# Performance work log

Hardware: AMD Instinct MI355X
Metric: run time of the kernel (lower is better)

## Reference

```python
import jax, jax.numpy as jnp
import numpy as np

B, S, D, E, H, K = 2, 2048, 1024, 8, 4096, 2


def setup_inputs() -> dict:
    key = jax.random.key(0)
    ks = jax.random.split(key, 7)
    sd = 1.0 / np.sqrt(D)
    sh = 1.0 / np.sqrt(H)
    return {
        "x": jax.random.normal(ks[0], (B, S, D), dtype=jnp.float32),
        "router_w": jax.random.uniform(ks[1], (D, E), jnp.float32, -sd, sd),
        "router_b": jnp.zeros((E,), jnp.float32),
        "w1": jax.random.uniform(ks[2], (E, D, H), jnp.float32, -sd, sd),
        "b1": jnp.zeros((E, H), jnp.float32),
        "w2": jax.random.uniform(ks[3], (E, H, D), jnp.float32, -sh, sh),
        "b2": jnp.zeros((E, D), jnp.float32),
    }


def reference(x, router_w, router_b, w1, b1, w2, b2):
    # Router: softmax over experts, then top-k and renormalize
    router_logits = jnp.einsum("bsd,de->bse", x, router_w) + router_b
    router_probs = jax.nn.softmax(router_logits, axis=-1)
    top_k_probs, top_k_indices = jax.lax.top_k(router_probs, K)  # [B,S,K]
    top_k_probs = top_k_probs / jnp.sum(top_k_probs, axis=-1, keepdims=True)

    # Dense all-expert FFN (Block assumed: Linear -> GELU -> Linear)
    h = jax.nn.gelu(jnp.einsum("bsd,edh->bseh", x, w1) + b1)  # [B,S,E,H]
    expert_outputs = jnp.einsum("bseh,ehd->bsed", h, w2) + b2  # [B,S,E,D]

    # Gather top-k experts per token and combine with renormalized probs
    idx = top_k_indices[..., None]  # [B,S,K,1]
    selected = jnp.take_along_axis(expert_outputs, idx, axis=2)  # [B,S,K,D]
    return jnp.sum(selected * top_k_probs[..., None], axis=2)  # [B,S,D]
```

## Files before the change

### kernel.cpp

```cpp
#include <hip/hip_runtime.h>
#include <hip/hip_bf16.h>

#define TOK   4096
#define DDIM  1024
#define NEXP  8
#define HDIM  4096
#define KSEL  2
#define NPAIR (TOK * KSEL)

typedef __attribute__((ext_vector_type(8))) _Float16 f16x8;
typedef __attribute__((ext_vector_type(4))) _Float16 f16x4;
typedef __attribute__((ext_vector_type(4))) float    f32x4;

__device__ __forceinline__ void gload16(const void* g, void* l) {
  __builtin_amdgcn_global_load_lds((const __attribute__((address_space(1))) void*)g,
                                   (__attribute__((address_space(3))) void*)l, 16, 0, 0);
}

__device__ __forceinline__ float gelu_tanh(float u) {
  float inner = 0.7978845608028654f * (u + 0.044715f * u * u * u);
  float t2 = __expf(2.f * inner);
  return u - u / (t2 + 1.f);
}

__global__ __launch_bounds__(256) void k_router(const float* __restrict__ x,
    const float* __restrict__ rw, const float* __restrict__ rb,
    int* __restrict__ tidx, float* __restrict__ tw, int* __restrict__ counts,
    _Float16* __restrict__ xb) {
  const int t    = blockIdx.x * 4 + (threadIdx.x >> 6);
  const int lane = threadIdx.x & 63;
  const float* xr = x + (size_t)t * DDIM;
  _Float16*   xbr = xb + (size_t)t * DDIM;
  float acc[NEXP];
#pragma unroll
  for (int e = 0; e < NEXP; ++e) acc[e] = 0.f;
  for (int d0 = lane * 4; d0 < DDIM; d0 += 256) {
    const float4 xv = *(const float4*)(xr + d0);
    f16x4 hx;
    hx[0] = (_Float16)xv.x; hx[1] = (_Float16)xv.y;
    hx[2] = (_Float16)xv.z; hx[3] = (_Float16)xv.w;
    *(f16x4*)(xbr + d0) = hx;
#pragma unroll
    for (int i = 0; i < 4; ++i) {
      const float xs = (&xv.x)[i];
      const float4 r0 = *(const float4*)(rw + (size_t)(d0 + i) * NEXP);
      const float4 r1 = *(const float4*)(rw + (size_t)(d0 + i) * NEXP + 4);
      acc[0] += xs * r0.x; acc[1] += xs * r0.y; acc[2] += xs * r0.z; acc[3] += xs * r0.w;
      acc[4] += xs * r1.x; acc[5] += xs * r1.y; acc[6] += xs * r1.z; acc[7] += xs * r1.w;
    }
  }
#pragma unroll
  for (int e = 0; e < NEXP; ++e) {
    float v = acc[e];
#pragma unroll
    for (int s = 32; s; s >>= 1) v += __shfl_xor(v, s, 64);
    acc[e] = v;
  }
  if (lane == 0) {
    float lg[NEXP];
#pragma unroll
    for (int e = 0; e < NEXP; ++e) lg[e] = acc[e] + rb[e];
    int i0 = 0;
#pragma unroll
    for (int e = 1; e < NEXP; ++e) if (lg[e] > lg[i0]) i0 = e;
    int i1 = -1; float best = -3.4e38f;
#pragma unroll
    for (int e = 0; e < NEXP; ++e) {
      if (e == i0) continue;
      if (lg[e] > best) { best = lg[e]; i1 = e; }
    }
    float w0 = 1.f / (1.f + expf(lg[i1] - lg[i0]));
    tidx[t * 2]     = i0;  tidx[t * 2 + 1] = i1;
    tw[t * 2]       = w0;  tw[t * 2 + 1]   = 1.f - w0;
    atomicAdd(&counts[i0], 1);
    atomicAdd(&counts[i1], 1);
  }
}

__global__ __launch_bounds__(1024) void k_scan(const int* __restrict__ tidx,
                       const float* __restrict__ tw,
                       const int* __restrict__ counts, int* __restrict__ offs,
                       int* __restrict__ row_token, float* __restrict__ row_w,
                       int* __restrict__ inv) {
  __shared__ int soff[NEXP + 1];
  __shared__ int scur[NEXP];
  if (threadIdx.x == 0) {
    int run = 0;
    for (int e = 0; e < NEXP; ++e) { soff[e] = run; run += counts[e]; }
    soff[NEXP] = run;
    for (int e = 0; e <= NEXP; ++e) offs[e] = soff[e];
  }
  __syncthreads();
  if (threadIdx.x < NEXP) scur[threadIdx.x] = soff[threadIdx.x];
  __syncthreads();
  const int lane = threadIdx.x & 63;
#pragma unroll
  for (int it = 0; it < NPAIR / 1024; ++it) {
    const int p = it * 1024 + threadIdx.x;
    const int e = tidx[p];
    int pos = 0;
#pragma unroll
    for (int ee = 0; ee < NEXP; ++ee) {
      unsigned long long m = __ballot(e == ee);
      if (!m) continue;
      int base = 0;
      if (lane == 0) base = atomicAdd(&scur[ee], __popcll(m));
      base = __shfl(base, 0, 64);
      if (e == ee) pos = base + __popcll(m & ((1ull << lane) - 1ull));
    }
    row_token[pos] = p >> 1;
    row_w[pos]     = tw[p];
    inv[p]         = pos;
  }
}

__global__ __launch_bounds__(256) void k_transpose(const float* __restrict__ in,
    _Float16* __restrict__ out, int Rr, int Cc) {
  __shared__ _Float16 tile[64][72];
  const size_t esz = (size_t)Rr * Cc;
  const float* ip = in + esz * blockIdx.z;
  _Float16*    op = out + esz * blockIdx.z;
  const int i0 = blockIdx.y * 64;
  const int j0 = blockIdx.x * 64;
  const int tx = threadIdx.x & 15, ty = threadIdx.x >> 4;
#pragma unroll
  for (int rr = 0; rr < 4; ++rr) {
    int r = ty + rr * 16;
    float4 v = *(const float4*)(ip + (size_t)(i0 + r) * Cc + j0 + tx * 4);
    tile[r][tx * 4 + 0] = (_Float16)v.x;
    tile[r][tx * 4 + 1] = (_Float16)v.y;
    tile[r][tx * 4 + 2] = (_Float16)v.z;
    tile[r][tx * 4 + 3] = (_Float16)v.w;
  }
  __syncthreads();
#pragma unroll
  for (int cc = 0; cc < 4; ++cc) {
    int c = ty + cc * 16;
    f16x4 o;
#pragma unroll
    for (int k = 0; k < 4; ++k) o[k] = tile[tx * 4 + k][c];
    *(f16x4*)(op + (size_t)(j0 + c) * Rr + i0 + tx * 4) = o;
  }
}

#define BM 128
#define BN 128
#define BKK 32


__global__ __launch_bounds__(256) void k_gemm1(
    const _Float16* __restrict__ xb,
    const _Float16* __restrict__ w1t,
    const float* __restrict__ b1,
    const int* __restrict__ offs,
    const int* __restrict__ row_token,
    _Float16* __restrict__ hbuf) {
  const int e    = blockIdx.z;
  const int off0 = offs[e];
  const int ne   = offs[e + 1] - off0;
  const int m0   = blockIdx.y * BM;
  if (m0 >= ne) return;
  const int n0   = blockIdx.x * BN;
  const int mrem = ne - m0;

  __shared__ __align__(16) char smem[32768];

  const int tid = threadIdx.x;
  const int wv = tid >> 6, lane = tid & 63;
  const int l15 = lane & 15;
  const int wr = wv >> 1, wc = wv & 1;

  const int rA0 = (wv * 2 + 0) * 16 + (lane >> 2);
  const int rA1 = (wv * 2 + 1) * 16 + (lane >> 2);
  const char* a_c = (const char*)xb;
  const char* b_c = (const char*)(w1t + (size_t)e * HDIM * DDIM);
  const int rc0 = (rA0 < mrem) ? rA0 : (mrem - 1);
  const int rc1 = (rA1 < mrem) ? rA1 : (mrem - 1);
  const char* ap0 = a_c + (size_t)row_token[off0 + m0 + rc0] * (DDIM * 2)
                        + (((lane & 3) ^ ((rA0 >> 1) & 3)) << 4);
  const char* ap1 = a_c + (size_t)row_token[off0 + m0 + rc1] * (DDIM * 2)
                        + (((lane & 3) ^ ((rA1 >> 1) & 3)) << 4);
  const char* bp0 = b_c + (size_t)(n0 + rA0) * (DDIM * 2)
                        + (((lane & 3) ^ ((rA0 >> 1) & 3)) << 4);
  const char* bp1 = b_c + (size_t)(n0 + rA1) * (DDIM * 2)
                        + (((lane & 3) ^ ((rA1 >> 1) & 3)) << 4);
  char* ldsA0 = smem + (wv * 2 + 0) * 1024;
  char* ldsA1 = smem + (wv * 2 + 1) * 1024;
  char* ldsB0 = smem + 16384 + (wv * 2 + 0) * 1024;
  char* ldsB1 = smem + 16384 + (wv * 2 + 1) * 1024;

  const unsigned foff = (unsigned)(((lane >> 4) ^ ((l15 >> 1) & 3)) << 4);

  f32x4 acc[4][4] = {};
  const int NT = DDIM / BKK;

  gload16(ap0, ldsA0); gload16(ap1, ldsA1);
  gload16(bp0, ldsB0); gload16(bp1, ldsB1);

#pragma unroll 2
  for (int ks = 0; ks < NT; ++ks) {
    const int cur = ks & 1;
    if (ks + 1 < NT) {
      const int nb = (cur ^ 1) * 8192;
      const size_t kb = (size_t)(ks + 1) * 64;
      gload16(ap0 + kb, ldsA0 + nb); gload16(ap1 + kb, ldsA1 + nb);
      gload16(bp0 + kb, ldsB0 + nb); gload16(bp1 + kb, ldsB1 + nb);
      asm volatile("s_waitcnt vmcnt(4)" ::: "memory");
    } else {
      asm volatile("s_waitcnt vmcnt(0)" ::: "memory");
    }
    __builtin_amdgcn_sched_barrier(0);
    __builtin_amdgcn_s_barrier();
    const char* Ab = smem + cur * 8192;
    const char* Bb = smem + 16384 + cur * 8192;
    f16x8 af[4], bfr[4];
#pragma unroll
    for (int m = 0; m < 4; ++m)
      af[m] = *(const f16x8*)(Ab + (wr * 64 + m * 16 + l15) * 64 + foff);
#pragma unroll
    for (int n = 0; n < 4; ++n)
      bfr[n] = *(const f16x8*)(Bb + (wc * 64 + n * 16 + l15) * 64 + foff);
#pragma unroll
    for (int m = 0; m < 4; ++m)
#pragma unroll
      for (int n = 0; n < 4; ++n)
        acc[m][n] = __builtin_amdgcn_mfma_f32_16x16x32_f16(af[m], bfr[n], acc[m][n], 0, 0, 0);
    __builtin_amdgcn_sched_barrier(0);
    __builtin_amdgcn_s_barrier();
  }

  float bias[4];
#pragma unroll
  for (int n = 0; n < 4; ++n)
    bias[n] = b1[(size_t)e * HDIM + n0 + wc * 64 + n * 16 + l15];
#pragma unroll
  for (int m = 0; m < 4; ++m) {
#pragma unroll
    for (int j = 0; j < 4; ++j) {
      int row = wr * 64 + m * 16 + (lane >> 4) * 4 + j;
#pragma unroll
      for (int n = 0; n < 4; ++n) {
        int col = wc * 64 + n * 16 + l15;
        *(_Float16*)(smem + (row << 8) + (((col << 1) ^ ((row & 15) << 4)))) =
            (_Float16)gelu_tanh(acc[m][n][j] + bias[n]);
      }
    }
  }
  __syncthreads();
  {
    const int srow = tid >> 1, half = tid & 1;
    if (srow < mrem) {
      _Float16* hr = hbuf + (size_t)(off0 + m0 + srow) * HDIM + n0 + half * 64;
#pragma unroll
      for (int i = 0; i < 8; ++i) {
        f16x8 v = *(const f16x8*)(smem + (srow << 8) + (((half * 128 + i * 16) ^ ((srow & 15) << 4))));
        *(f16x8*)(hr + i * 8) = v;
      }
    }
  }
}

template <bool YB>
__global__ __launch_bounds__(256) void k_gemm2(
    const _Float16* __restrict__ hbuf,
    const _Float16* __restrict__ w2t,
    const float* __restrict__ b2,
    const int* __restrict__ offs,
    const int* __restrict__ row_token,
    const float* __restrict__ row_w,
    _Float16* __restrict__ yb,
    float* __restrict__ out) {
  const int e    = blockIdx.z >> 1;
  const int kh   = blockIdx.z & 1;
  const int off0 = offs[e];
  const int ne   = offs[e + 1] - off0;
  const int m0   = blockIdx.y * BM;
  if (m0 >= ne) return;
  const int n0   = blockIdx.x * BN;
  const int mrem = ne - m0;

  __shared__ __align__(16) char smem[32768];

  const int tid = threadIdx.x;
  const int wv = tid >> 6, lane = tid & 63;
  const int l15 = lane & 15;
  const int wr = wv >> 1, wc = wv & 1;

  const int rA0 = (wv * 2 + 0) * 16 + (lane >> 2);
  const int rA1 = (wv * 2 + 1) * 16 + (lane >> 2);
  const char* a_c = (const char*)hbuf;
  const char* b_c = (const char*)(w2t + (size_t)e * DDIM * HDIM);
  const int rc0 = (rA0 < mrem) ? rA0 : (mrem - 1);
  const int rc1 = (rA1 < mrem) ? rA1 : (mrem - 1);
  const size_t khb = (size_t)kh * (2048 * 2);
  const char* ap0 = a_c + (size_t)(off0 + m0 + rc0) * (HDIM * 2) + khb
                        + (((lane & 3) ^ ((rA0 >> 1) & 3)) << 4);
  const char* ap1 = a_c + (size_t)(off0 + m0 + rc1) * (HDIM * 2) + khb
                        + (((lane & 3) ^ ((rA1 >> 1) & 3)) << 4);
  const char* bp0 = b_c + (size_t)(n0 + rA0) * (HDIM * 2) + khb
                        + (((lane & 3) ^ ((rA0 >> 1) & 3)) << 4);
  const char* bp1 = b_c + (size_t)(n0 + rA1) * (HDIM * 2) + khb
                        + (((lane & 3) ^ ((rA1 >> 1) & 3)) << 4);
  char* ldsA0 = smem + (wv * 2 + 0) * 1024;
  char* ldsA1 = smem + (wv * 2 + 1) * 1024;
  char* ldsB0 = smem + 16384 + (wv * 2 + 0) * 1024;
  char* ldsB1 = smem + 16384 + (wv * 2 + 1) * 1024;

  const unsigned foff = (unsigned)(((lane >> 4) ^ ((l15 >> 1) & 3)) << 4);

  f32x4 acc[4][4] = {};
  const int NT = 2048 / BKK;

  gload16(ap0, ldsA0); gload16(ap1, ldsA1);
  gload16(bp0, ldsB0); gload16(bp1, ldsB1);

#pragma unroll 2
  for (int ks = 0; ks < NT; ++ks) {
    const int cur = ks & 1;
    if (ks + 1 < NT) {
      const int nb = (cur ^ 1) * 8192;
      const size_t kb = (size_t)(ks + 1) * 64;
      gload16(ap0 + kb, ldsA0 + nb); gload16(ap1 + kb, ldsA1 + nb);
      gload16(bp0 + kb, ldsB0 + nb); gload16(bp1 + kb, ldsB1 + nb);
      asm volatile("s_waitcnt vmcnt(4)" ::: "memory");
    } else {
      asm volatile("s_waitcnt vmcnt(0)" ::: "memory");
    }
    __builtin_amdgcn_sched_barrier(0);
    __builtin_amdgcn_s_barrier();
    const char* Ab = smem + cur * 8192;
    const char* Bb = smem + 16384 + cur * 8192;
    f16x8 af[4], bfr[4];
#pragma unroll
    for (int m = 0; m < 4; ++m)
      af[m] = *(const f16x8*)(Ab + (wr * 64 + m * 16 + l15) * 64 + foff);
#pragma unroll
    for (int n = 0; n < 4; ++n)
      bfr[n] = *(const f16x8*)(Bb + (wc * 64 + n * 16 + l15) * 64 + foff);
#pragma unroll
    for (int m = 0; m < 4; ++m)
#pragma unroll
      for (int n = 0; n < 4; ++n)
        acc[m][n] = __builtin_amdgcn_mfma_f32_16x16x32_f16(af[m], bfr[n], acc[m][n], 0, 0, 0);
    __builtin_amdgcn_sched_barrier(0);
    __builtin_amdgcn_s_barrier();
  }

  if (YB) {
    _Float16* ypart = yb + (size_t)kh * NPAIR * DDIM;
#pragma unroll
    for (int m = 0; m < 4; ++m) {
#pragma unroll
      for (int j = 0; j < 4; ++j) {
        int row = wr * 64 + m * 16 + (lane >> 4) * 4 + j;
#pragma unroll
        for (int n = 0; n < 4; ++n) {
          int col = wc * 64 + n * 16 + l15;
          *(_Float16*)(smem + (row << 8) + (((col << 1) ^ ((row & 15) << 4)))) =
              (_Float16)acc[m][n][j];
        }
      }
    }
    __syncthreads();
    const int srow = tid >> 1, half = tid & 1;
    if (srow < mrem) {
      _Float16* yr = ypart + (size_t)(off0 + m0 + srow) * DDIM + n0 + half * 64;
#pragma unroll
      for (int i = 0; i < 8; ++i) {
        f16x8 v = *(const f16x8*)(smem + (srow << 8) + (((half * 128 + i * 16) ^ ((srow & 15) << 4))));
        *(f16x8*)(yr + i * 8) = v;
      }
    }
  } else {
    float bias[4];
#pragma unroll
    for (int n = 0; n < 4; ++n)
      bias[n] = (kh == 0) ? b2[(size_t)e * DDIM + n0 + wc * 64 + n * 16 + l15] : 0.f;
#pragma unroll
    for (int m = 0; m < 4; ++m) {
#pragma unroll
      for (int j = 0; j < 4; ++j) {
        int row = wr * 64 + m * 16 + (lane >> 4) * 4 + j;
        if (row < mrem) {
          int g = off0 + m0 + row;
          float wgt = row_w[g];
          float* op = out + (size_t)row_token[g] * DDIM + n0 + wc * 64 + l15;
#pragma unroll
          for (int n = 0; n < 4; ++n)
            atomicAdd(op + n * 16, wgt * (acc[m][n][j] + bias[n]));
        }
      }
    }
  }
}

__global__ __launch_bounds__(256) void k_combine(const _Float16* __restrict__ yb,
    const int* __restrict__ inv, const int* __restrict__ tidx,
    const float* __restrict__ tw, const float* __restrict__ b2,
    float* __restrict__ out) {
  const int t  = blockIdx.x * 2 + (threadIdx.x >> 7);
  const int c8 = (threadIdx.x & 127) * 8;
  const int g0 = inv[2 * t],  g1 = inv[2 * t + 1];
  const int e0 = tidx[2 * t], e1 = tidx[2 * t + 1];
  const float w0 = tw[2 * t], w1 = tw[2 * t + 1];
  const _Float16* y1p = yb + (size_t)NPAIR * DDIM;
  f16x8 a0 = *(const f16x8*)(yb  + (size_t)g0 * DDIM + c8);
  f16x8 a1 = *(const f16x8*)(y1p + (size_t)g0 * DDIM + c8);
  f16x8 b0 = *(const f16x8*)(yb  + (size_t)g1 * DDIM + c8);
  f16x8 b1v = *(const f16x8*)(y1p + (size_t)g1 * DDIM + c8);
  float o[8];
#pragma unroll
  for (int i = 0; i < 8; ++i) {
    float bA = b2[(size_t)e0 * DDIM + c8 + i];
    float bB = b2[(size_t)e1 * DDIM + c8 + i];
    o[i] = w0 * ((float)a0[i] + (float)a1[i] + bA) + w1 * ((float)b0[i] + (float)b1v[i] + bB);
  }
  float* op = out + (size_t)t * DDIM + c8;
  *(float4*)op       = make_float4(o[0], o[1], o[2], o[3]);
  *(float4*)(op + 4) = make_float4(o[4], o[5], o[6], o[7]);
}

extern "C" void kernel_launch(void* const* d_in, const int* in_sizes, int n_in,
                              void* d_out, int out_size, void* d_ws, size_t ws_size,
                              hipStream_t stream) {
  const float* x  = (const float*)d_in[0];
  const float* rw = (const float*)d_in[1];
  const float* rb = (const float*)d_in[2];
  const float* w1 = (const float*)d_in[3];
  const float* b1 = (const float*)d_in[4];
  const float* w2 = (const float*)d_in[5];
  const float* b2 = (const float*)d_in[6];
  float* out = (float*)d_out;
  char* ws = (char*)d_ws;

  int*      tidx    = (int*)(ws + 0);
  float*    tw      = (float*)(ws + 32768);
  int*      counts  = (int*)(ws + 65536);
  int*      offs    = (int*)(ws + 65792);
  int*      row_tok = (int*)(ws + 66048);
  float*    row_w   = (float*)(ws + 98816);
  int*      inv     = (int*)(ws + 131584);
  _Float16* xb      = (_Float16*)(ws + 164352);
  _Float16* wt      = (_Float16*)(ws + 8552960);
  _Float16* hb      = (_Float16*)(ws + 75661824);
  _Float16* yb      = (_Float16*)(ws + 142770688);
  const bool big = ws_size >= 209879552ULL;

  hipMemsetAsync(counts, 0, NEXP * sizeof(int), stream);
  if (!big) hipMemsetAsync(out, 0, (size_t)TOK * DDIM * sizeof(float), stream);

  k_router<<<dim3(TOK / 4), 256, 0, stream>>>(x, rw, rb, tidx, tw, counts, xb);
  k_scan<<<dim3(1), 1024, 0, stream>>>(tidx, tw, counts, offs, row_tok, row_w, inv);
  k_transpose<<<dim3(HDIM / 64, DDIM / 64, NEXP), 256, 0, stream>>>(w1, wt, DDIM, HDIM);
  k_gemm1<<<dim3(HDIM / BN, TOK / BM, NEXP), 256, 0, stream>>>(xb, wt, b1, offs, row_tok, hb);
  k_transpose<<<dim3(DDIM / 64, HDIM / 64, NEXP), 256, 0, stream>>>(w2, wt, HDIM, DDIM);
  if (big) {
    k_gemm2<true><<<dim3(DDIM / BN, TOK / BM, NEXP * 2), 256, 0, stream>>>(
        hb, wt, b2, offs, row_tok, row_w, yb, out);
    k_combine<<<dim3(TOK / 2), 256, 0, stream>>>(yb, inv, tidx, tw, b2, out);
  } else {
    k_gemm2<false><<<dim3(DDIM / BN, TOK / BM, NEXP * 2), 256, 0, stream>>>(
        hb, wt, b2, offs, row_tok, row_w, yb, out);
  }
}
```

Baseline: 427.3 us.

## Triple-buffer GEMM K-loop prefetch and remap grid to 1D with N-outer ordering

Both grouped GEMM kernels move from double-buffered to triple-buffered LDS staging. Loads run two K-steps ahead and wait with vmcnt(8), giving more global-memory latency hiding at the cost of 48KB LDS per block, which may reduce occupancy. The 3D grid is flattened to 1D and decoded so consecutive blocks cover all M tiles and experts for one N tile. This changes the block schedule so weight tiles are reused from L2 more often. Early-exit blocks for empty M tiles are now interleaved in the launch order.

```diff
diff --git a/kernel.cpp b/kernel.cpp
--- a/kernel.cpp
+++ b/kernel.cpp
@@ -155,15 +155,19 @@
     const int* __restrict__ offs,
     const int* __restrict__ row_token,
     _Float16* __restrict__ hbuf) {
-  const int e    = blockIdx.z;
+  const int id = blockIdx.x;
+  const int nx = id >> 8;
+  const int r_ = id & 255;
+  const int my = r_ & 31;
+  const int e  = r_ >> 5;
   const int off0 = offs[e];
   const int ne   = offs[e + 1] - off0;
-  const int m0   = blockIdx.y * BM;
+  const int m0   = my * BM;
   if (m0 >= ne) return;
-  const int n0   = blockIdx.x * BN;
+  const int n0   = nx * BN;
   const int mrem = ne - m0;
 
-  __shared__ __align__(16) char smem[32768];
+  __shared__ __align__(16) char smem[49152];
 
   const int tid = threadIdx.x;
   const int wv = tid >> 6, lane = tid & 63;
@@ -184,35 +188,37 @@
                         + (((lane & 3) ^ ((rA0 >> 1) & 3)) << 4);
   const char* bp1 = b_c + (size_t)(n0 + rA1) * (DDIM * 2)
                         + (((lane & 3) ^ ((rA1 >> 1) & 3)) << 4);
-  char* ldsA0 = smem + (wv * 2 + 0) * 1024;
-  char* ldsA1 = smem + (wv * 2 + 1) * 1024;
-  char* ldsB0 = smem + 16384 + (wv * 2 + 0) * 1024;
-  char* ldsB1 = smem + 16384 + (wv * 2 + 1) * 1024;
+  char* ldsA = smem;
+  char* ldsB = smem + 24576;
+  const int ch0 = (wv * 2 + 0) * 1024, ch1 = (wv * 2 + 1) * 1024;
 
   const unsigned foff = (unsigned)(((lane >> 4) ^ ((l15 >> 1) & 3)) << 4);
 
   f32x4 acc[4][4] = {};
   const int NT = DDIM / BKK;
 
-  gload16(ap0, ldsA0); gload16(ap1, ldsA1);
-  gload16(bp0, ldsB0); gload16(bp1, ldsB1);
-
-#pragma unroll 2
+  gload16(ap0, ldsA + ch0);        gload16(ap1, ldsA + ch1);
+  gload16(bp0, ldsB + ch0);        gload16(bp1, ldsB + ch1);
+  gload16(ap0 + 64, ldsA + 8192 + ch0); gload16(ap1 + 64, ldsA + 8192 + ch1);
+  gload16(bp0 + 64, ldsB + 8192 + ch0); gload16(bp1 + 64, ldsB + 8192 + ch1);
+
+  int cur = 0, nx2 = 2;
   for (int ks = 0; ks < NT; ++ks) {
-    const int cur = ks & 1;
-    if (ks + 1 < NT) {
-      const int nb = (cur ^ 1) * 8192;
-      const size_t kb = (size_t)(ks + 1) * 64;
-      gload16(ap0 + kb, ldsA0 + nb); gload16(ap1 + kb, ldsA1 + nb);
-      gload16(bp0 + kb, ldsB0 + nb); gload16(bp1 + kb, ldsB1 + nb);
+    if (ks + 2 < NT) {
+      const size_t kb = (size_t)(ks + 2) * 64;
+      const int nb = nx2 * 8192;
+      gload16(ap0 + kb, ldsA + nb + ch0); gload16(ap1 + kb, ldsA + nb + ch1);
+      gload16(bp0 + kb, ldsB + nb + ch0); gload16(bp1 + kb, ldsB + nb + ch1);
+      asm volatile("s_waitcnt vmcnt(8)" ::: "memory");
+    } else if (ks + 1 < NT) {
       asm volatile("s_waitcnt vmcnt(4)" ::: "memory");
     } else {
       asm volatile("s_waitcnt vmcnt(0)" ::: "memory");
     }
     __builtin_amdgcn_sched_barrier(0);
     __builtin_amdgcn_s_barrier();
-    const char* Ab = smem + cur * 8192;
-    const char* Bb = smem + 16384 + cur * 8192;
+    const char* Ab = ldsA + cur * 8192;
+    const char* Bb = ldsB + cur * 8192;
     f16x8 af[4], bfr[4];
 #pragma unroll
     for (int m = 0; m < 4; ++m)
@@ -227,6 +233,8 @@
         acc[m][n] = __builtin_amdgcn_mfma_f32_16x16x32_f16(af[m], bfr[n], acc[m][n], 0, 0, 0);
     __builtin_amdgcn_sched_barrier(0);
     __builtin_amdgcn_s_barrier();
+    cur = (cur == 2) ? 0 : cur + 1;
+    nx2 = (nx2 == 2) ? 0 : nx2 + 1;
   }
 
   float bias[4];
@@ -270,16 +278,21 @@
     const float* __restrict__ row_w,
     _Float16* __restrict__ yb,
     float* __restrict__ out) {
-  const int e    = blockIdx.z >> 1;
-  const int kh   = blockIdx.z & 1;
+  const int id = blockIdx.x;
+  const int nx = id >> 9;
+  const int r_ = id & 511;
+  const int my = r_ & 31;
+  const int zz = r_ >> 5;
+  const int e  = zz >> 1;
+  const int kh = zz & 1;
   const int off0 = offs[e];
   const int ne   = offs[e + 1] - off0;
-  const int m0   = blockIdx.y * BM;
+  const int m0   = my * BM;
   if (m0 >= ne) return;
-  const int n0   = blockIdx.x * BN;
+  const int n0   = nx * BN;
   const int mrem = ne - m0;
 
-  __shared__ __align__(16) char smem[32768];
+  __shared__ __align__(16) char smem[49152];
 
   const int tid = threadIdx.x;
   const int wv = tid >> 6, lane = tid & 63;
@@ -301,35 +314,37 @@
                         + (((lane & 3) ^ ((rA0 >> 1) & 3)) << 4);
   const char* bp1 = b_c + (size_t)(n0 + rA1) * (HDIM * 2) + khb
                         + (((lane & 3) ^ ((rA1 >> 1) & 3)) << 4);
-  char* ldsA0 = smem + (wv * 2 + 0) * 1024;
-  char* ldsA1 = smem + (wv * 2 + 1) * 1024;
-  char* ldsB0 = smem + 16384 + (wv * 2 + 0) * 1024;
-  char* ldsB1 = smem + 16384 + (wv * 2 + 1) * 1024;
+  char* ldsA = smem;
+  char* ldsB = smem + 24576;
+  const int ch0 = (wv * 2 + 0) * 1024, ch1 = (wv * 2 + 1) * 1024;
 
   const unsigned foff = (unsigned)(((lane >> 4) ^ ((l15 >> 1) & 3)) << 4);
 
   f32x4 acc[4][4] = {};
   const int NT = 2048 / BKK;
 
-  gload16(ap0, ldsA0); gload16(ap1, ldsA1);
-  gload16(bp0, ldsB0); gload16(bp1, ldsB1);
-
-#pragma unroll 2
+  gload16(ap0, ldsA + ch0);        gload16(ap1, ldsA + ch1);
+  gload16(bp0, ldsB + ch0);        gload16(bp1, ldsB + ch1);
+  gload16(ap0 + 64, ldsA + 8192 + ch0); gload16(ap1 + 64, ldsA + 8192 + ch1);
+  gload16(bp0 + 64, ldsB + 8192 + ch0); gload16(bp1 + 64, ldsB + 8192 + ch1);
+
+  int cur = 0, nx2 = 2;
   for (int ks = 0; ks < NT; ++ks) {
-    const int cur = ks & 1;
-    if (ks + 1 < NT) {
-      const int nb = (cur ^ 1) * 8192;
-      const size_t kb = (size_t)(ks + 1) * 64;
-      gload16(ap0 + kb, ldsA0 + nb); gload16(ap1 + kb, ldsA1 + nb);
-      gload16(bp0 + kb, ldsB0 + nb); gload16(bp1 + kb, ldsB1 + nb);
+    if (ks + 2 < NT) {
+      const size_t kb = (size_t)(ks + 2) * 64;
+      const int nb = nx2 * 8192;
+      gload16(ap0 + kb, ldsA + nb + ch0); gload16(ap1 + kb, ldsA + nb + ch1);
+      gload16(bp0 + kb, ldsB + nb + ch0); gload16(bp1 + kb, ldsB + nb + ch1);
+      asm volatile("s_waitcnt vmcnt(8)" ::: "memory");
+    } else if (ks + 1 < NT) {
       asm volatile("s_waitcnt vmcnt(4)" ::: "memory");
     } else {
       asm volatile("s_waitcnt vmcnt(0)" ::: "memory");
     }
     __builtin_amdgcn_sched_barrier(0);
     __builtin_amdgcn_s_barrier();
-    const char* Ab = smem + cur * 8192;
-    const char* Bb = smem + 16384 + cur * 8192;
+    const char* Ab = ldsA + cur * 8192;
+    const char* Bb = ldsB + cur * 8192;
     f16x8 af[4], bfr[4];
 #pragma unroll
     for (int m = 0; m < 4; ++m)
@@ -344,6 +359,8 @@
         acc[m][n] = __builtin_amdgcn_mfma_f32_16x16x32_f16(af[m], bfr[n], acc[m][n], 0, 0, 0);
     __builtin_amdgcn_sched_barrier(0);
     __builtin_amdgcn_s_barrier();
+    cur = (cur == 2) ? 0 : cur + 1;
+    nx2 = (nx2 == 2) ? 0 : nx2 + 1;
   }
 
   if (YB) {
@@ -452,14 +469,14 @@
   k_router<<<dim3(TOK / 4), 256, 0, stream>>>(x, rw, rb, tidx, tw, counts, xb);
   k_scan<<<dim3(1), 1024, 0, stream>>>(tidx, tw, counts, offs, row_tok, row_w, inv);
   k_transpose<<<dim3(HDIM / 64, DDIM / 64, NEXP), 256, 0, stream>>>(w1, wt, DDIM, HDIM);
-  k_gemm1<<<dim3(HDIM / BN, TOK / BM, NEXP), 256, 0, stream>>>(xb, wt, b1, offs, row_tok, hb);
+  k_gemm1<<<dim3((HDIM / BN) * (TOK / BM) * NEXP), 256, 0, stream>>>(xb, wt, b1, offs, row_tok, hb);
   k_transpose<<<dim3(DDIM / 64, HDIM / 64, NEXP), 256, 0, stream>>>(w2, wt, HDIM, DDIM);
   if (big) {
-    k_gemm2<true><<<dim3(DDIM / BN, TOK / BM, NEXP * 2), 256, 0, stream>>>(
+    k_gemm2<true><<<dim3((DDIM / BN) * (TOK / BM) * NEXP * 2), 256, 0, stream>>>(
         hb, wt, b2, offs, row_tok, row_w, yb, out);
     k_combine<<<dim3(TOK / 2), 256, 0, stream>>>(yb, inv, tidx, tw, b2, out);
   } else {
-    k_gemm2<false><<<dim3(DDIM / BN, TOK / BM, NEXP * 2), 256, 0, stream>>>(
+    k_gemm2<false><<<dim3((DDIM / BN) * (TOK / BM) * NEXP * 2), 256, 0, stream>>>(
         hb, wt, b2, offs, row_tok, row_w, yb, out);
   }
 }
```

After: 843.3 us. 97.4% more time.
